# Optimization experiments

Measured on AMD Instinct MI355X. Metric: run time of the kernel, lower is better.

Reference implementation:

```python
import jax, jax.numpy as jnp
import numpy as np

N = 100000      # nodes
E = 3200000     # edges (avg degree 32)
T = 5           # time slices / periods
F_IN = 10       # num_node_features
HID = 16        # hidden_channels
C = 2           # num_classes


def setup_inputs() -> dict:
    key = jax.random.key(0)
    ks = jax.random.split(key, 16)
    rn = lambda k, s: (jax.random.normal(k, s, dtype=jnp.float32) * 0.1)
    z = lambda s: jnp.zeros(s, dtype=jnp.float32)
    return {
        'x': jax.random.normal(ks[0], (T, N, F_IN), dtype=jnp.float32),
        'src': jax.random.randint(ks[1], (E,), 0, N, dtype=jnp.int32),
        'dst': jax.random.randint(ks[2], (E,), 0, N, dtype=jnp.int32),
        'W1': rn(ks[3], (F_IN, HID)), 'b1': z((HID,)),
        'W2': rn(ks[4], (HID, HID)), 'b2': z((HID,)),
        'Wz': rn(ks[5], (HID, HID)), 'bz': z((HID,)),
        'Wr': rn(ks[6], (HID, HID)), 'br': z((HID,)),
        'Wh': rn(ks[7], (HID, HID)), 'bh': z((HID,)),
        'Lz': rn(ks[8], (2 * HID, HID)), 'lz': z((HID,)),
        'Lr': rn(ks[9], (2 * HID, HID)), 'lr': z((HID,)),
        'Lh': rn(ks[10], (2 * HID, HID)), 'lh': z((HID,)),
        'att': rn(ks[11], (T,)),
        'fcW': rn(ks[12], (HID, C)), 'fcb': z((C,)),
    }


def reference(x, src, dst, W1, b1, W2, b2, Wz, bz, Wr, br, Wh, bh,
              Lz, lz, Lr, lr, Lh, lh, att, fcW, fcb):
    n = x.shape[1]
    # symmetric GCN normalization with self-loops (PyG gcn_norm)
    deg = jax.ops.segment_sum(jnp.ones_like(src, dtype=x.dtype), dst,
                              num_segments=n) + 1.0
    dis = jax.lax.rsqrt(deg)
    enorm = dis[src] * dis[dst]          # [E]
    deg_inv = 1.0 / deg                  # self-loop weight d^-1

    def gcn(h, W, b):
        hw = h @ W                                                   # [n,out]
        agg = jax.ops.segment_sum(enorm[:, None] * hw[src], dst,
                                  num_segments=n)
        return agg + deg_inv[:, None] * hw + b

    # two stacked GCN layers per time slice (shared weights, vmapped over T)
    def per_slice(xt):
        h = jax.nn.relu(gcn(xt, W1, b1))
        return jax.nn.relu(gcn(h, W2, b2))

    feats = jax.vmap(per_slice)(x)       # [T, n, HID]

    # TGCN (GRU with GCNConv gates) unrolled over periods
    def cell(Hst, xt):
        Zg = jax.nn.sigmoid(jnp.concatenate([gcn(xt, Wz, bz), Hst], axis=1) @ Lz + lz)
        Rg = jax.nn.sigmoid(jnp.concatenate([gcn(xt, Wr, br), Hst], axis=1) @ Lr + lr)
        Ht = jnp.tanh(jnp.concatenate([gcn(xt, Wh, bh), Hst * Rg], axis=1) @ Lh + lh)
        Hnew = Zg * Hst + (1.0 - Zg) * Ht
        return Hnew, Hnew

    H0 = jnp.zeros((n, HID), dtype=x.dtype)
    _, Hs = jax.lax.scan(cell, H0, feats)            # [T, n, HID]

    # A3TGCN attention-weighted accumulation over periods
    probs = jax.nn.softmax(att)
    Hacc = jnp.einsum('t,tnh->nh', probs, Hs)        # [n, HID]

    logits = Hacc @ fcW + fcb                        # [n, C]
    return jax.nn.log_softmax(logits, axis=1)
```

## Files before the change

### kernel.cpp

```cpp
#include <hip/hip_runtime.h>
#include <hip/hip_bf16.h>

typedef unsigned int u32;
typedef unsigned short u16;

struct WPtrs { const void* p[19]; };


__device__ __forceinline__ float sigm(float x){ return 1.0f/(1.0f+__expf(-x)); }

__device__ __forceinline__ float bflo(u32 u){ return __uint_as_float(u << 16); }
__device__ __forceinline__ float bfhi(u32 u){ return __uint_as_float(u & 0xffff0000u); }
__device__ __forceinline__ u32 packbf(float a, float b){
    u32 ua = __float_as_uint(a), ub = __float_as_uint(b);
    ua += 0x7fffu + ((ua >> 16) & 1u);
    ub += 0x7fffu + ((ub >> 16) & 1u);
    return (ua >> 16) | (ub & 0xffff0000u);
}

__global__ __launch_bounds__(256)
void k_prep(const void* __restrict__ x, WPtrs wp, int* __restrict__ flagp,
            float* __restrict__ wsW)
{
    __shared__ int scount;
    __shared__ int sflag;
    if (threadIdx.x == 0) scount = 0;
    __syncthreads();
    const u16* xs = (const u16*)x;
    int cnt = 0;
    #pragma unroll
    for (int j = 0; j < 8; j++) {
        int k = (threadIdx.x*8 + j) * 1201;
        u16 u = xs[2*k];
        int ex = (u >> 7) & 0xFF;
        cnt += (ex >= 110 && ex <= 140) ? 1 : 0;
    }
    atomicAdd(&scount, cnt);
    __syncthreads();
    if (threadIdx.x == 0) { sflag = (scount > 1024) ? 1 : 0; flagp[0] = sflag; }
    __syncthreads();
    const int flag = sflag;

    const int sizes[19] = {160,16,256,16,256,16,256,16,256,16,512,16,512,16,512,16,5,32,2};
    int off = 0;
    for (int a = 0; a < 19; a++) {
        const void* s = wp.p[a];
        for (int j = threadIdx.x; j < sizes[a]; j += 256) {
            float v = flag ? __bfloat162float(((const __hip_bfloat16*)s)[j])
                           : ((const float*)s)[j];
            wsW[off + j] = v;
        }
        off += sizes[a];
    }
    __syncthreads();
    {
        int k = threadIdx.x >> 4, j = threadIdx.x & 15;
        float az = 0.f, ar = 0.f, ah = 0.f;
        #pragma unroll
        for (int m = 0; m < 16; m++) {
            az += wsW[448 + k*16 + m] * wsW[1264 + m*16 + j];
            ar += wsW[720 + k*16 + m] * wsW[1792 + m*16 + j];
            ah += wsW[992 + k*16 + m] * wsW[2320 + m*16 + j];
        }
        wsW[2944 + threadIdx.x] = az;
        wsW[3200 + threadIdx.x] = ar;
        wsW[3456 + threadIdx.x] = ah;
        if (threadIdx.x < 16) {
            float cz = wsW[1776 + j], cr = wsW[2304 + j], ch = wsW[2832 + j];
            #pragma unroll
            for (int m = 0; m < 16; m++) {
                cz += wsW[704  + m] * wsW[1264 + m*16 + j];
                cr += wsW[976  + m] * wsW[1792 + m*16 + j];
                ch += wsW[1248 + m] * wsW[2320 + m*16 + j];
            }
            wsW[3712 + j] = cz; wsW[3728 + j] = cr; wsW[3744 + j] = ch;
        }
    }
    __syncthreads();
    {
        int j = threadIdx.x;
        wsW[4096 +        j] = wsW[2944 + j];
        wsW[4096 +  256 + j] = wsW[3200 + j];
        wsW[4096 +  512 + j] = wsW[3456 + j];
        wsW[4096 +  768 + j] = wsW[1520 + j];
        wsW[4096 + 1024 + j] = wsW[2048 + j];
        wsW[4096 + 1280 + j] = wsW[2576 + j];
        if (j < 16) {
            wsW[4096 + 1536 + j] = wsW[3712 + j];
            wsW[4096 + 1552 + j] = wsW[3728 + j];
            wsW[4096 + 1568 + j] = wsW[3744 + j];
        }
        if (j < 32) wsW[4096 + 1592 + j] = wsW[2853 + j];
        if (j < 2)  wsW[4096 + 1624 + j] = wsW[2885 + j];
        if (j == 0) {
            float a0=wsW[2848],a1=wsW[2849],a2=wsW[2850],a3=wsW[2851],a4=wsW[2852];
            float am = fmaxf(fmaxf(fmaxf(a0,a1),fmaxf(a2,a3)),a4);
            float e0=__expf(a0-am),e1=__expf(a1-am),e2=__expf(a2-am),
                  e3=__expf(a3-am),e4=__expf(a4-am);
            float inv = 1.f/(e0+e1+e2+e3+e4);
            wsW[4096+1584+0]=e0*inv; wsW[4096+1584+1]=e1*inv;
            wsW[4096+1584+2]=e2*inv; wsW[4096+1584+3]=e3*inv;
            wsW[4096+1584+4]=e4*inv;
        }
    }
}

__global__ __launch_bounds__(256)
void k_deg(const int* __restrict__ dst, int* __restrict__ deg, int E)
{
    int e = blockIdx.x*256 + threadIdx.x;
    if (e < E) atomicAdd(&deg[dst[e]], 1);
}

__global__ __launch_bounds__(256)
void k_scan_a(const int* __restrict__ deg, float* __restrict__ dis,
              float* __restrict__ dinv, int* __restrict__ bsum, int N)
{
    __shared__ int sm[256];
    int i = blockIdx.x*256 + threadIdx.x;
    int c = (i < N) ? deg[i] : 0;
    if (i < N) {
        float d = (float)(c + 1);
        dis[i]  = rsqrtf(d);
        dinv[i] = 1.0f / d;
    }
    sm[threadIdx.x] = c; __syncthreads();
    for (int s = 128; s > 0; s >>= 1) {
        if (threadIdx.x < s) sm[threadIdx.x] += sm[threadIdx.x + s];
        __syncthreads();
    }
    if (threadIdx.x == 0) bsum[blockIdx.x] = sm[0];
}

__global__ void k_scan_b(const int* __restrict__ bsum, int* __restrict__ boff, int nb)
{
    __shared__ int sm[512];
    int t = threadIdx.x;
    int v = (t < nb) ? bsum[t] : 0;
    sm[t] = v; __syncthreads();
    for (int s = 1; s < 512; s <<= 1) {
        int add = (t >= s) ? sm[t - s] : 0;
        __syncthreads();
        sm[t] += add;
        __syncthreads();
    }
    if (t < nb) boff[t] = sm[t] - v;
}

__global__ __launch_bounds__(256)
void k_scan_c(const int* __restrict__ deg, const int* __restrict__ boff,
              int* __restrict__ row_start, int* __restrict__ cursor, int N, int E)
{
    __shared__ int sm[256];
    int t = threadIdx.x;
    int i = blockIdx.x*256 + t;
    int c = (i < N) ? deg[i] : 0;
    sm[t] = c; __syncthreads();
    for (int s = 1; s < 256; s <<= 1) {
        int add = (t >= s) ? sm[t - s] : 0;
        __syncthreads();
        sm[t] += add;
        __syncthreads();
    }
    int rs = boff[blockIdx.x] + sm[t] - c;
    if (i < N) {
        row_start[i] = rs;
        cursor[i]    = rs;
        if (i == N - 1) row_start[N] = rs + c;
    }
}

__global__ __launch_bounds__(256)
void k_fill(const int* __restrict__ src, const int* __restrict__ dst,
            const float* __restrict__ dis, int* __restrict__ cursor,
            int2* __restrict__ csr, int E)
{
    int e = blockIdx.x*256 + threadIdx.x;
    if (e < E) {
        int s = src[e], d = dst[e];
        int pos = atomicAdd(&cursor[d], 1);
        csr[pos] = make_int2(s, __float_as_int(dis[s]));
    }
}

__global__ __launch_bounds__(256)
void k_g1(const void* __restrict__ x, const int* __restrict__ flagp,
          const float* __restrict__ dis, const float* __restrict__ dinv,
          const int* __restrict__ row_start, const int2* __restrict__ csr,
          const float* __restrict__ wsW, u32* __restrict__ B, int N)
{
    __shared__ float w[176];
    for (int j = threadIdx.x; j < 176; j += 256) w[j] = wsW[j];
    __syncthreads();
    int tid = blockIdx.x*256 + threadIdx.x;
    if (tid >= N*5) return;
    int i = tid / 5, t = tid - i*5;
    const int flag = flagp[0];

    float acc[10];
    float dd = dis[i], di = dinv[i];
    int rs = row_start[i], re = row_start[i+1];
    size_t selfb = ((size_t)t*N + i)*5;

    if (flag) {
        const u32* xb = (const u32*)x;
        #pragma unroll
        for (int m = 0; m < 5; m++) {
            u32 u = xb[selfb + m];
            acc[2*m]   = di*bflo(u);
            acc[2*m+1] = di*bfhi(u);
        }
        int k = rs;
        for (; k + 1 < re; k += 2) {
            int2 sw0 = csr[k], sw1 = csr[k+1];
            float wg0 = dd * __int_as_float(sw0.y);
            float wg1 = dd * __int_as_float(sw1.y);
            size_t b0 = ((size_t)t*N + sw0.x)*5;
            size_t b1 = ((size_t)t*N + sw1.x)*5;
            #pragma unroll
            for (int m = 0; m < 5; m++) {
                u32 u0 = xb[b0 + m], u1 = xb[b1 + m];
                acc[2*m]   += wg0*bflo(u0) + wg1*bflo(u1);
                acc[2*m+1] += wg0*bfhi(u0) + wg1*bfhi(u1);
            }
        }
        if (k < re) {
            int2 sw = csr[k];
            float wg = dd * __int_as_float(sw.y);
            size_t b = ((size_t)t*N + sw.x)*5;
            #pragma unroll
            for (int m = 0; m < 5; m++) {
                u32 u = xb[b + m];
                acc[2*m]   += wg*bflo(u);
                acc[2*m+1] += wg*bfhi(u);
            }
        }
    } else {
        const float2* xf = (const float2*)x;
        #pragma unroll
        for (int m = 0; m < 5; m++) {
            float2 f2 = xf[selfb + m];
            acc[2*m]   = di*f2.x;
            acc[2*m+1] = di*f2.y;
        }
        int k = rs;
        for (; k + 1 < re; k += 2) {
            int2 sw0 = csr[k], sw1 = csr[k+1];
            float wg0 = dd * __int_as_float(sw0.y);
            float wg1 = dd * __int_as_float(sw1.y);
            size_t b0 = ((size_t)t*N + sw0.x)*5;
            size_t b1 = ((size_t)t*N + sw1.x)*5;
            #pragma unroll
            for (int m = 0; m < 5; m++) {
                float2 f0 = xf[b0 + m], f1 = xf[b1 + m];
                acc[2*m]   += wg0*f0.x + wg1*f1.x;
                acc[2*m+1] += wg0*f0.y + wg1*f1.y;
            }
        }
        if (k < re) {
            int2 sw = csr[k];
            float wg = dd * __int_as_float(sw.y);
            size_t b = ((size_t)t*N + sw.x)*5;
            #pragma unroll
            for (int m = 0; m < 5; m++) {
                float2 f2 = xf[b + m];
                acc[2*m]   += wg*f2.x;
                acc[2*m+1] += wg*f2.y;
            }
        }
    }

    float hh[16];
    #pragma unroll
    for (int jb = 0; jb < 4; jb++) {
        float4 h = ((const float4*)&w[160])[jb];
        #pragma unroll
        for (int f = 0; f < 10; f++) {
            float4 wv = ((const float4*)w)[f*4 + jb];
            h.x += acc[f]*wv.x; h.y += acc[f]*wv.y;
            h.z += acc[f]*wv.z; h.w += acc[f]*wv.w;
        }
        hh[jb*4+0] = fmaxf(h.x, 0.f); hh[jb*4+1] = fmaxf(h.y, 0.f);
        hh[jb*4+2] = fmaxf(h.z, 0.f); hh[jb*4+3] = fmaxf(h.w, 0.f);
    }
    u32* orow = B + (size_t)i*40 + t*8;
    uint4 o0 = make_uint4(packbf(hh[0],hh[1]), packbf(hh[2],hh[3]),
                          packbf(hh[4],hh[5]), packbf(hh[6],hh[7]));
    uint4 o1 = make_uint4(packbf(hh[8],hh[9]), packbf(hh[10],hh[11]),
                          packbf(hh[12],hh[13]), packbf(hh[14],hh[15]));
    ((uint4*)orow)[0] = o0;
    ((uint4*)orow)[1] = o1;
}

__device__ __forceinline__ void acc_chunk(const u32* __restrict__ p, float wg,
                                          float* __restrict__ acc)
{
    uint4 a = ((const uint4*)p)[0];
    uint4 b = ((const uint4*)p)[1];
    acc[0] += wg*bflo(a.x); acc[1] += wg*bfhi(a.x);
    acc[2] += wg*bflo(a.y); acc[3] += wg*bfhi(a.y);
    acc[4] += wg*bflo(a.z); acc[5] += wg*bfhi(a.z);
    acc[6] += wg*bflo(a.w); acc[7] += wg*bfhi(a.w);
    acc[8]  += wg*bflo(b.x); acc[9]  += wg*bfhi(b.x);
    acc[10] += wg*bflo(b.y); acc[11] += wg*bfhi(b.y);
    acc[12] += wg*bflo(b.z); acc[13] += wg*bfhi(b.z);
    acc[14] += wg*bflo(b.w); acc[15] += wg*bfhi(b.w);
}

__global__ __launch_bounds__(256)
void k_g2(const u32* __restrict__ Fin, const float* __restrict__ dis,
          const float* __restrict__ dinv, const int* __restrict__ row_start,
          const int2* __restrict__ csr, const float* __restrict__ wsW,
          u32* __restrict__ B, int N)
{
    __shared__ float w[272];
    for (int j = threadIdx.x; j < 272; j += 256) w[j] = wsW[176 + j];
    __syncthreads();
    int tid = blockIdx.x*256 + threadIdx.x;
    if (tid >= N*5) return;
    int i = tid / 5, t = tid - i*5;

    float dd = dis[i], di = dinv[i];
    int rs = row_start[i], re = row_start[i+1];

    float acc[16];
    #pragma unroll
    for (int j = 0; j < 16; j++) acc[j] = 0.f;
    acc_chunk(Fin + (size_t)i*40 + t*8, di, acc);

    int k = rs;
    for (; k + 1 < re; k += 2) {
        int2 sw0 = csr[k], sw1 = csr[k+1];
        acc_chunk(Fin + (size_t)sw0.x*40 + t*8, dd*__int_as_float(sw0.y), acc);
        acc_chunk(Fin + (size_t)sw1.x*40 + t*8, dd*__int_as_float(sw1.y), acc);
    }
    if (k < re) {
        int2 sw = csr[k];
        acc_chunk(Fin + (size_t)sw.x*40 + t*8, dd*__int_as_float(sw.y), acc);
    }

    float hh[16];
    #pragma unroll
    for (int jb = 0; jb < 4; jb++) {
        float4 h = ((const float4*)&w[256])[jb];
        #pragma unroll
        for (int f = 0; f < 16; f++) {
            float4 wv = ((const float4*)w)[f*4 + jb];
            h.x += acc[f]*wv.x; h.y += acc[f]*wv.y;
            h.z += acc[f]*wv.z; h.w += acc[f]*wv.w;
        }
        hh[jb*4+0] = fmaxf(h.x, 0.f); hh[jb*4+1] = fmaxf(h.y, 0.f);
        hh[jb*4+2] = fmaxf(h.z, 0.f); hh[jb*4+3] = fmaxf(h.w, 0.f);
    }
    u32* orow = B + (size_t)i*40 + t*8;
    uint4 o0 = make_uint4(packbf(hh[0],hh[1]), packbf(hh[2],hh[3]),
                          packbf(hh[4],hh[5]), packbf(hh[6],hh[7]));
    uint4 o1 = make_uint4(packbf(hh[8],hh[9]), packbf(hh[10],hh[11]),
                          packbf(hh[12],hh[13]), packbf(hh[14],hh[15]));
    ((uint4*)orow)[0] = o0;
    ((uint4*)orow)[1] = o1;
}

__global__ __launch_bounds__(256)
void k_g3(const u32* __restrict__ Fin, const float* __restrict__ dis,
          const float* __restrict__ dinv, const int* __restrict__ row_start,
          const int2* __restrict__ csr, u32* __restrict__ B, int N)
{
    int tid = blockIdx.x*256 + threadIdx.x;
    if (tid >= N*5) return;
    int i = tid / 5, t = tid - i*5;

    float dd = dis[i], di = dinv[i];
    int rs = row_start[i], re = row_start[i+1];

    float acc[16];
    #pragma unroll
    for (int j = 0; j < 16; j++) acc[j] = 0.f;
    acc_chunk(Fin + (size_t)i*40 + t*8, di, acc);

    int k = rs;
    for (; k + 1 < re; k += 2) {
        int2 sw0 = csr[k], sw1 = csr[k+1];
        acc_chunk(Fin + (size_t)sw0.x*40 + t*8, dd*__int_as_float(sw0.y), acc);
        acc_chunk(Fin + (size_t)sw1.x*40 + t*8, dd*__int_as_float(sw1.y), acc);
    }
    if (k < re) {
        int2 sw = csr[k];
        acc_chunk(Fin + (size_t)sw.x*40 + t*8, dd*__int_as_float(sw.y), acc);
    }

    u32* orow = B + (size_t)i*40 + t*8;
    uint4 o0 = make_uint4(packbf(acc[0],acc[1]), packbf(acc[2],acc[3]),
                          packbf(acc[4],acc[5]), packbf(acc[6],acc[7]));
    uint4 o1 = make_uint4(packbf(acc[8],acc[9]), packbf(acc[10],acc[11]),
                          packbf(acc[12],acc[13]), packbf(acc[14],acc[15]));
    ((uint4*)orow)[0] = o0;
    ((uint4*)orow)[1] = o1;
}

__global__ __launch_bounds__(256)
void k_gru(const u32* __restrict__ C, const float* __restrict__ wsW,
           const int* __restrict__ flagp, void* __restrict__ out, int N)
{
    __shared__ __align__(16) float sm[1632];
    for (int j = threadIdx.x; j < 1632; j += 256) sm[j] = wsW[4096 + j];
    __syncthreads();

    int i = blockIdx.x*256 + threadIdx.x;
    if (i >= N) return;

    const float4* Az = (const float4*)&sm[0];
    const float4* Ar = (const float4*)&sm[256];
    const float4* Ah = (const float4*)&sm[512];
    const float4* Lz = (const float4*)&sm[768];
    const float4* Lr = (const float4*)&sm[1024];
    const float4* Lh = (const float4*)&sm[1280];

    float H[16];
    #pragma unroll
    for (int j = 0; j < 16; j++) H[j] = 0.f;
    float z0 = sm[1624], z1 = sm[1625];

    for (int t = 0; t < 5; t++) {
        float pf[16];
        {
            const u32* p = C + (size_t)i*40 + t*8;
            uint4 a = ((const uint4*)p)[0];
            uint4 b = ((const uint4*)p)[1];
            pf[0]=bflo(a.x); pf[1]=bfhi(a.x); pf[2]=bflo(a.y); pf[3]=bfhi(a.y);
            pf[4]=bflo(a.z); pf[5]=bfhi(a.z); pf[6]=bflo(a.w); pf[7]=bfhi(a.w);
            pf[8]=bflo(b.x); pf[9]=bfhi(b.x); pf[10]=bflo(b.y); pf[11]=bfhi(b.y);
            pf[12]=bflo(b.z); pf[13]=bfhi(b.z); pf[14]=bflo(b.w); pf[15]=bfhi(b.w);
        }

        float Zg[16];
        #pragma unroll
        for (int jb = 0; jb < 4; jb++) {
            float4 a = ((const float4*)&sm[1536])[jb];
            #pragma unroll
            for (int k = 0; k < 16; k++) {
                float pp = pf[k]; float4 wv = Az[k*4+jb];
                a.x += pp*wv.x; a.y += pp*wv.y; a.z += pp*wv.z; a.w += pp*wv.w;
            }
            #pragma unroll
            for (int k = 0; k < 16; k++) {
                float h = H[k]; float4 wv = Lz[k*4+jb];
                a.x += h*wv.x; a.y += h*wv.y; a.z += h*wv.z; a.w += h*wv.w;
            }
            Zg[jb*4+0]=sigm(a.x); Zg[jb*4+1]=sigm(a.y);
            Zg[jb*4+2]=sigm(a.z); Zg[jb*4+3]=sigm(a.w);
        }
        float HR[16];
        #pragma unroll
        for (int jb = 0; jb < 4; jb++) {
            float4 a = ((const float4*)&sm[1552])[jb];
            #pragma unroll
            for (int k = 0; k < 16; k++) {
                float pp = pf[k]; float4 wv = Ar[k*4+jb];
                a.x += pp*wv.x; a.y += pp*wv.y; a.z += pp*wv.z; a.w += pp*wv.w;
            }
            #pragma unroll
            for (int k = 0; k < 16; k++) {
                float h = H[k]; float4 wv = Lr[k*4+jb];
                a.x += h*wv.x; a.y += h*wv.y; a.z += h*wv.z; a.w += h*wv.w;
            }
            HR[jb*4+0]=H[jb*4+0]*sigm(a.x); HR[jb*4+1]=H[jb*4+1]*sigm(a.y);
            HR[jb*4+2]=H[jb*4+2]*sigm(a.z); HR[jb*4+3]=H[jb*4+3]*sigm(a.w);
        }
        #pragma unroll
        for (int jb = 0; jb < 4; jb++) {
            float4 a = ((const float4*)&sm[1568])[jb];
            #pragma unroll
            for (int k = 0; k < 16; k++) {
                float pp = pf[k]; float4 wv = Ah[k*4+jb];
                a.x += pp*wv.x; a.y += pp*wv.y; a.z += pp*wv.z; a.w += pp*wv.w;
            }
            #pragma unroll
            for (int k = 0; k < 16; k++) {
                float h = HR[k]; float4 wv = Lh[k*4+jb];
                a.x += h*wv.x; a.y += h*wv.y; a.z += h*wv.z; a.w += h*wv.w;
            }
            #pragma unroll
            for (int q = 0; q < 4; q++) {
                int j = jb*4 + q;
                float v = (q==0)?a.x:(q==1)?a.y:(q==2)?a.z:a.w;
                v = fminf(fmaxf(v, -15.f), 15.f);
                float ex = __expf(2.f*v);
                float th = (ex - 1.f) / (ex + 1.f);
                float z = Zg[j];
                H[j] = z*H[j] + (1.f - z)*th;
            }
        }
        float pr = sm[1584 + t];
        float s0 = 0.f, s1 = 0.f;
        #pragma unroll
        for (int k = 0; k < 16; k++) {
            s0 += H[k]*sm[1592 + k*2];
            s1 += H[k]*sm[1592 + k*2 + 1];
        }
        z0 += pr*s0; z1 += pr*s1;
    }

    float mm = fmaxf(z0, z1);
    float l  = __logf(__expf(z0-mm) + __expf(z1-mm));
    float o0 = z0 - mm - l, o1 = z1 - mm - l;
    if (flagp[0]) {
        ((u32*)out)[i] = packbf(o0, o1);
    } else {
        ((float2*)out)[i] = make_float2(o0, o1);
    }
}

__global__ void k_tail(const int* __restrict__ flagp, const int* __restrict__ deg,
                       int* __restrict__ sink)
{
    if (threadIdx.x == 0) sink[0] = flagp[0] + deg[0];
}

extern "C" void kernel_launch(void* const* d_in, const int* in_sizes, int n_in,
                              void* d_out, int out_size, void* d_ws, size_t ws_size,
                              hipStream_t stream)
{
    const void* x   = d_in[0];
    const int* src  = (const int*)d_in[1];
    const int* dst  = (const int*)d_in[2];
    int N = in_sizes[0] / 50;
    int E = in_sizes[1];

    char* ws = (char*)d_ws;
    size_t off = 0;
    auto alloc = [&](size_t bytes) -> void* {
        void* p = ws + off;
        off = (off + bytes + 255) & ~(size_t)255;
        return p;
    };
    int*   flagp     = (int*)  alloc(64);
    int*   sink      = (int*)  alloc(64);
    float* wsW       = (float*)alloc(8192*4);
    int*   deg       = (int*)  alloc((size_t)N*4);
    float* dis       = (float*)alloc((size_t)N*4);
    float* dinv      = (float*)alloc((size_t)N*4);
    int*   row_start = (int*)  alloc(((size_t)N+1)*4);
    int*   cursor    = (int*)  alloc((size_t)N*4);
    int*   bsum      = (int*)  alloc(4096);
    int*   boff      = (int*)  alloc(4096);
    int2*  csr       = (int2*) alloc((size_t)E*8);
    u32*   bufA      = (u32*)  alloc((size_t)N*40*4);
    u32*   bufB      = (u32*)  alloc((size_t)N*40*4);
    u32*   bufC      = (u32*)  alloc((size_t)N*40*4);

    int nb  = (N + 255) / 256;
    int gE  = (E + 255) / 256;
    int g5  = ((size_t)N*5 + 255) / 256;

    hipMemsetAsync(deg, 0, (size_t)N*4, stream);

    WPtrs wp;
    for (int a = 0; a < 19; a++) wp.p[a] = d_in[3 + a];
    k_prep<<<1, 256, 0, stream>>>(x, wp, flagp, wsW);

    k_deg   <<<gE, 256, 0, stream>>>(dst, deg, E);
    k_scan_a<<<nb, 256, 0, stream>>>(deg, dis, dinv, bsum, N);
    k_scan_b<<<1, 512, 0, stream>>>(bsum, boff, nb);
    k_scan_c<<<nb, 256, 0, stream>>>(deg, boff, row_start, cursor, N, E);
    k_fill  <<<gE, 256, 0, stream>>>(src, dst, dis, cursor, csr, E);

    k_g1 <<<g5, 256, 0, stream>>>(x, flagp, dis, dinv, row_start, csr, wsW, bufA, N);
    k_g2 <<<g5, 256, 0, stream>>>(bufA, dis, dinv, row_start, csr, wsW, bufB, N);
    k_g3 <<<g5, 256, 0, stream>>>(bufB, dis, dinv, row_start, csr, bufC, N);
    k_gru<<<nb, 256, 0, stream>>>(bufC, wsW, flagp, d_out, N);
    k_tail<<<1, 64, 0, stream>>>(flagp, deg, sink);
}
```

Measured before the change: 2.351 ms.

## Fuse third GCN aggregation with GRU recurrence via shared memory

Merges the third graph aggregation kernel with the GRU/attention/log-softmax kernel. Each block handles 51 nodes times 5 time slices, stages the fp32 aggregates in shared memory, and then 51 threads run the recurrence. This removes the bufC round trip through global memory, one launch, and the bf16 rounding of that intermediate. It also drops the tail kernel. The cost is that the GRU phase uses only 51 of 256 threads per block, and the larger shared memory footprint may reduce occupancy.

```diff
diff --git a/kernel.cpp b/kernel.cpp
--- a/kernel.cpp
+++ b/kernel.cpp
@@ -362,159 +362,150 @@
 }
 
 __global__ __launch_bounds__(256)
-void k_g3(const u32* __restrict__ Fin, const float* __restrict__ dis,
-          const float* __restrict__ dinv, const int* __restrict__ row_start,
-          const int2* __restrict__ csr, u32* __restrict__ B, int N)
-{
-    int tid = blockIdx.x*256 + threadIdx.x;
-    if (tid >= N*5) return;
-    int i = tid / 5, t = tid - i*5;
-
-    float dd = dis[i], di = dinv[i];
-    int rs = row_start[i], re = row_start[i+1];
-
-    float acc[16];
-    #pragma unroll
-    for (int j = 0; j < 16; j++) acc[j] = 0.f;
-    acc_chunk(Fin + (size_t)i*40 + t*8, di, acc);
-
-    int k = rs;
-    for (; k + 1 < re; k += 2) {
-        int2 sw0 = csr[k], sw1 = csr[k+1];
-        acc_chunk(Fin + (size_t)sw0.x*40 + t*8, dd*__int_as_float(sw0.y), acc);
-        acc_chunk(Fin + (size_t)sw1.x*40 + t*8, dd*__int_as_float(sw1.y), acc);
-    }
-    if (k < re) {
-        int2 sw = csr[k];
-        acc_chunk(Fin + (size_t)sw.x*40 + t*8, dd*__int_as_float(sw.y), acc);
-    }
-
-    u32* orow = B + (size_t)i*40 + t*8;
-    uint4 o0 = make_uint4(packbf(acc[0],acc[1]), packbf(acc[2],acc[3]),
-                          packbf(acc[4],acc[5]), packbf(acc[6],acc[7]));
-    uint4 o1 = make_uint4(packbf(acc[8],acc[9]), packbf(acc[10],acc[11]),
-                          packbf(acc[12],acc[13]), packbf(acc[14],acc[15]));
-    ((uint4*)orow)[0] = o0;
-    ((uint4*)orow)[1] = o1;
-}
-
-__global__ __launch_bounds__(256)
-void k_gru(const u32* __restrict__ C, const float* __restrict__ wsW,
-           const int* __restrict__ flagp, void* __restrict__ out, int N)
-{
-    __shared__ __align__(16) float sm[1632];
-    for (int j = threadIdx.x; j < 1632; j += 256) sm[j] = wsW[4096 + j];
-    __syncthreads();
-
-    int i = blockIdx.x*256 + threadIdx.x;
-    if (i >= N) return;
-
-    const float4* Az = (const float4*)&sm[0];
-    const float4* Ar = (const float4*)&sm[256];
-    const float4* Ah = (const float4*)&sm[512];
-    const float4* Lz = (const float4*)&sm[768];
-    const float4* Lr = (const float4*)&sm[1024];
-    const float4* Lh = (const float4*)&sm[1280];
-
-    float H[16];
-    #pragma unroll
-    for (int j = 0; j < 16; j++) H[j] = 0.f;
-    float z0 = sm[1624], z1 = sm[1625];
-
-    for (int t = 0; t < 5; t++) {
-        float pf[16];
-        {
-            const u32* p = C + (size_t)i*40 + t*8;
-            uint4 a = ((const uint4*)p)[0];
-            uint4 b = ((const uint4*)p)[1];
-            pf[0]=bflo(a.x); pf[1]=bfhi(a.x); pf[2]=bflo(a.y); pf[3]=bfhi(a.y);
-            pf[4]=bflo(a.z); pf[5]=bfhi(a.z); pf[6]=bflo(a.w); pf[7]=bfhi(a.w);
-            pf[8]=bflo(b.x); pf[9]=bfhi(b.x); pf[10]=bflo(b.y); pf[11]=bfhi(b.y);
-            pf[12]=bflo(b.z); pf[13]=bfhi(b.z); pf[14]=bflo(b.w); pf[15]=bfhi(b.w);
-        }
-
-        float Zg[16];
-        #pragma unroll
-        for (int jb = 0; jb < 4; jb++) {
-            float4 a = ((const float4*)&sm[1536])[jb];
+void k_g3gru(const u32* __restrict__ Fin, const float* __restrict__ dis,
+             const float* __restrict__ dinv, const int* __restrict__ row_start,
+             const int2* __restrict__ csr, const float* __restrict__ wsW,
+             const int* __restrict__ flagp, void* __restrict__ out, int N)
+{
+    __shared__ __align__(16) float smW[1632];
+    __shared__ __align__(16) float smP[255*16];
+    for (int j = threadIdx.x; j < 1632; j += 256) smW[j] = wsW[4096 + j];
+
+    const int tid = threadIdx.x;
+    const int i0  = blockIdx.x * 51;
+    const int nl  = tid / 5;
+    const int t   = tid - nl*5;
+    const int i   = i0 + nl;
+
+    if (tid < 255 && i < N) {
+        float dd = dis[i], di = dinv[i];
+        int rs = row_start[i], re = row_start[i+1];
+
+        float acc[16];
+        #pragma unroll
+        for (int j = 0; j < 16; j++) acc[j] = 0.f;
+        acc_chunk(Fin + (size_t)i*40 + t*8, di, acc);
+
+        int k = rs;
+        for (; k + 1 < re; k += 2) {
+            int2 sw0 = csr[k], sw1 = csr[k+1];
+            acc_chunk(Fin + (size_t)sw0.x*40 + t*8, dd*__int_as_float(sw0.y), acc);
+            acc_chunk(Fin + (size_t)sw1.x*40 + t*8, dd*__int_as_float(sw1.y), acc);
+        }
+        if (k < re) {
+            int2 sw = csr[k];
+            acc_chunk(Fin + (size_t)sw.x*40 + t*8, dd*__int_as_float(sw.y), acc);
+        }
+        float4* prow = (float4*)&smP[tid*16];
+        prow[0] = make_float4(acc[0],acc[1],acc[2],acc[3]);
+        prow[1] = make_float4(acc[4],acc[5],acc[6],acc[7]);
+        prow[2] = make_float4(acc[8],acc[9],acc[10],acc[11]);
+        prow[3] = make_float4(acc[12],acc[13],acc[14],acc[15]);
+    }
+    __syncthreads();
+
+    if (tid < 51 && i0 + tid < N) {
+        const int node = i0 + tid;
+        const float4* Az = (const float4*)&smW[0];
+        const float4* Ar = (const float4*)&smW[256];
+        const float4* Ah = (const float4*)&smW[512];
+        const float4* Lz = (const float4*)&smW[768];
+        const float4* Lr = (const float4*)&smW[1024];
+        const float4* Lh = (const float4*)&smW[1280];
+
+        float H[16];
+        #pragma unroll
+        for (int j = 0; j < 16; j++) H[j] = 0.f;
+        float z0 = smW[1624], z1 = smW[1625];
+
+        for (int tt = 0; tt < 5; tt++) {
+            float pf[16];
+            {
+                const float4* prow = (const float4*)&smP[(tid*5 + tt)*16];
+                float4 v0 = prow[0], v1 = prow[1], v2 = prow[2], v3 = prow[3];
+                pf[0]=v0.x; pf[1]=v0.y; pf[2]=v0.z; pf[3]=v0.w;
+                pf[4]=v1.x; pf[5]=v1.y; pf[6]=v1.z; pf[7]=v1.w;
+                pf[8]=v2.x; pf[9]=v2.y; pf[10]=v2.z; pf[11]=v2.w;
+                pf[12]=v3.x; pf[13]=v3.y; pf[14]=v3.z; pf[15]=v3.w;
+            }
+
+            float Zg[16];
+            #pragma unroll
+            for (int jb = 0; jb < 4; jb++) {
+                float4 a = ((const float4*)&smW[1536])[jb];
+                #pragma unroll
+                for (int k = 0; k < 16; k++) {
+                    float pp = pf[k]; float4 wv = Az[k*4+jb];
+                    a.x += pp*wv.x; a.y += pp*wv.y; a.z += pp*wv.z; a.w += pp*wv.w;
+                }
+                #pragma unroll
+                for (int k = 0; k < 16; k++) {
+                    float h = H[k]; float4 wv = Lz[k*4+jb];
+                    a.x += h*wv.x; a.y += h*wv.y; a.z += h*wv.z; a.w += h*wv.w;
+                }
+                Zg[jb*4+0]=sigm(a.x); Zg[jb*4+1]=sigm(a.y);
+                Zg[jb*4+2]=sigm(a.z); Zg[jb*4+3]=sigm(a.w);
+            }
+            float HR[16];
+            #pragma unroll
+            for (int jb = 0; jb < 4; jb++) {
+                float4 a = ((const float4*)&smW[1552])[jb];
+                #pragma unroll
+                for (int k = 0; k < 16; k++) {
+                    float pp = pf[k]; float4 wv = Ar[k*4+jb];
+                    a.x += pp*wv.x; a.y += pp*wv.y; a.z += pp*wv.z; a.w += pp*wv.w;
+                }
+                #pragma unroll
+                for (int k = 0; k < 16; k++) {
+                    float h = H[k]; float4 wv = Lr[k*4+jb];
+                    a.x += h*wv.x; a.y += h*wv.y; a.z += h*wv.z; a.w += h*wv.w;
+                }
+                HR[jb*4+0]=H[jb*4+0]*sigm(a.x); HR[jb*4+1]=H[jb*4+1]*sigm(a.y);
+                HR[jb*4+2]=H[jb*4+2]*sigm(a.z); HR[jb*4+3]=H[jb*4+3]*sigm(a.w);
+            }
+            #pragma unroll
+            for (int jb = 0; jb < 4; jb++) {
+                float4 a = ((const float4*)&smW[1568])[jb];
+                #pragma unroll
+                for (int k = 0; k < 16; k++) {
+                    float pp = pf[k]; float4 wv = Ah[k*4+jb];
+                    a.x += pp*wv.x; a.y += pp*wv.y; a.z += pp*wv.z; a.w += pp*wv.w;
+                }
+                #pragma unroll
+                for (int k = 0; k < 16; k++) {
+                    float h = HR[k]; float4 wv = Lh[k*4+jb];
+                    a.x += h*wv.x; a.y += h*wv.y; a.z += h*wv.z; a.w += h*wv.w;
+                }
+                #pragma unroll
+                for (int q = 0; q < 4; q++) {
+                    int j = jb*4 + q;
+                    float v = (q==0)?a.x:(q==1)?a.y:(q==2)?a.z:a.w;
+                    v = fminf(fmaxf(v, -15.f), 15.f);
+                    float ex = __expf(2.f*v);
+                    float th = (ex - 1.f) / (ex + 1.f);
+                    float z = Zg[j];
+                    H[j] = z*H[j] + (1.f - z)*th;
+                }
+            }
+            float pr = smW[1584 + tt];
+            float s0 = 0.f, s1 = 0.f;
             #pragma unroll
             for (int k = 0; k < 16; k++) {
-                float pp = pf[k]; float4 wv = Az[k*4+jb];
-                a.x += pp*wv.x; a.y += pp*wv.y; a.z += pp*wv.z; a.w += pp*wv.w;
-            }
-            #pragma unroll
-            for (int k = 0; k < 16; k++) {
-                float h = H[k]; float4 wv = Lz[k*4+jb];
-                a.x += h*wv.x; a.y += h*wv.y; a.z += h*wv.z; a.w += h*wv.w;
-            }
-            Zg[jb*4+0]=sigm(a.x); Zg[jb*4+1]=sigm(a.y);
-            Zg[jb*4+2]=sigm(a.z); Zg[jb*4+3]=sigm(a.w);
-        }
-        float HR[16];
-        #pragma unroll
-        for (int jb = 0; jb < 4; jb++) {
-            float4 a = ((const float4*)&sm[1552])[jb];
-            #pragma unroll
-            for (int k = 0; k < 16; k++) {
-                float pp = pf[k]; float4 wv = Ar[k*4+jb];
-                a.x += pp*wv.x; a.y += pp*wv.y; a.z += pp*wv.z; a.w += pp*wv.w;
-            }
-            #pragma unroll
-            for (int k = 0; k < 16; k++) {
-                float h = H[k]; float4 wv = Lr[k*4+jb];
-                a.x += h*wv.x; a.y += h*wv.y; a.z += h*wv.z; a.w += h*wv.w;
-            }
-            HR[jb*4+0]=H[jb*4+0]*sigm(a.x); HR[jb*4+1]=H[jb*4+1]*sigm(a.y);
-            HR[jb*4+2]=H[jb*4+2]*sigm(a.z); HR[jb*4+3]=H[jb*4+3]*sigm(a.w);
-        }
-        #pragma unroll
-        for (int jb = 0; jb < 4; jb++) {
-            float4 a = ((const float4*)&sm[1568])[jb];
-            #pragma unroll
-            for (int k = 0; k < 16; k++) {
-                float pp = pf[k]; float4 wv = Ah[k*4+jb];
-                a.x += pp*wv.x; a.y += pp*wv.y; a.z += pp*wv.z; a.w += pp*wv.w;
-            }
-            #pragma unroll
-            for (int k = 0; k < 16; k++) {
-                float h = HR[k]; float4 wv = Lh[k*4+jb];
-                a.x += h*wv.x; a.y += h*wv.y; a.z += h*wv.z; a.w += h*wv.w;
-            }
-            #pragma unroll
-            for (int q = 0; q < 4; q++) {
-                int j = jb*4 + q;
-                float v = (q==0)?a.x:(q==1)?a.y:(q==2)?a.z:a.w;
-                v = fminf(fmaxf(v, -15.f), 15.f);
-                float ex = __expf(2.f*v);
-                float th = (ex - 1.f) / (ex + 1.f);
-                float z = Zg[j];
-                H[j] = z*H[j] + (1.f - z)*th;
-            }
-        }
-        float pr = sm[1584 + t];
-        float s0 = 0.f, s1 = 0.f;
-        #pragma unroll
-        for (int k = 0; k < 16; k++) {
-            s0 += H[k]*sm[1592 + k*2];
-            s1 += H[k]*sm[1592 + k*2 + 1];
-        }
-        z0 += pr*s0; z1 += pr*s1;
-    }
-
-    float mm = fmaxf(z0, z1);
-    float l  = __logf(__expf(z0-mm) + __expf(z1-mm));
-    float o0 = z0 - mm - l, o1 = z1 - mm - l;
-    if (flagp[0]) {
-        ((u32*)out)[i] = packbf(o0, o1);
-    } else {
-        ((float2*)out)[i] = make_float2(o0, o1);
-    }
-}
-
-__global__ void k_tail(const int* __restrict__ flagp, const int* __restrict__ deg,
-                       int* __restrict__ sink)
-{
-    if (threadIdx.x == 0) sink[0] = flagp[0] + deg[0];
+                s0 += H[k]*smW[1592 + k*2];
+                s1 += H[k]*smW[1592 + k*2 + 1];
+            }
+            z0 += pr*s0; z1 += pr*s1;
+        }
+
+        float mm = fmaxf(z0, z1);
+        float l  = __logf(__expf(z0-mm) + __expf(z1-mm));
+        float o0 = z0 - mm - l, o1 = z1 - mm - l;
+        if (flagp[0]) {
+            ((u32*)out)[node] = packbf(o0, o1);
+        } else {
+            ((float2*)out)[node] = make_float2(o0, o1);
+        }
+    }
 }
 
 extern "C" void kernel_launch(void* const* d_in, const int* in_sizes, int n_in,
@@ -535,7 +526,6 @@
         return p;
     };
     int*   flagp     = (int*)  alloc(64);
-    int*   sink      = (int*)  alloc(64);
     float* wsW       = (float*)alloc(8192*4);
     int*   deg       = (int*)  alloc((size_t)N*4);
     float* dis       = (float*)alloc((size_t)N*4);
@@ -547,11 +537,11 @@
     int2*  csr       = (int2*) alloc((size_t)E*8);
     u32*   bufA      = (u32*)  alloc((size_t)N*40*4);
     u32*   bufB      = (u32*)  alloc((size_t)N*40*4);
-    u32*   bufC      = (u32*)  alloc((size_t)N*40*4);
 
     int nb  = (N + 255) / 256;
     int gE  = (E + 255) / 256;
     int g5  = ((size_t)N*5 + 255) / 256;
+    int g51 = (N + 50) / 51;
 
     hipMemsetAsync(deg, 0, (size_t)N*4, stream);
 
@@ -565,9 +555,8 @@
     k_scan_c<<<nb, 256, 0, stream>>>(deg, boff, row_start, cursor, N, E);
     k_fill  <<<gE, 256, 0, stream>>>(src, dst, dis, cursor, csr, E);
 
-    k_g1 <<<g5, 256, 0, stream>>>(x, flagp, dis, dinv, row_start, csr, wsW, bufA, N);
-    k_g2 <<<g5, 256, 0, stream>>>(bufA, dis, dinv, row_start, csr, wsW, bufB, N);
-    k_g3 <<<g5, 256, 0, stream>>>(bufB, dis, dinv, row_start, csr, bufC, N);
-    k_gru<<<nb, 256, 0, stream>>>(bufC, wsW, flagp, d_out, N);
-    k_tail<<<1, 64, 0, stream>>>(flagp, deg, sink);
-}
+    k_g1   <<<g5,  256, 0, stream>>>(x, flagp, dis, dinv, row_start, csr, wsW, bufA, N);
+    k_g2   <<<g5,  256, 0, stream>>>(bufA, dis, dinv, row_start, csr, wsW, bufB, N);
+    k_g3gru<<<g51, 256, 0, stream>>>(bufB, dis, dinv, row_start, csr, wsW, flagp,
+                                     d_out, N);
+}
```

Result: slower. 4.303 ms (+83.0%).
